# Kernel optimization log

Hardware: AMD Instinct MI355X
Metric: run time of the kernel (lower is better)

Reference implementation:

```python
import jax, jax.numpy as jnp
import numpy as np

ATTN_MULT = 8.0
NEG_INF = float('-inf')

N, Q, S, D = 16, 2048, 2048, 64


def setup_inputs() -> dict:
    key = jax.random.key(0)
    kq, kk, kv, kp = jax.random.split(key, 4)
    return {
        "queries_nqd": jax.random.normal(kq, (N, Q, D), dtype=jnp.float32),
        "keys_nsd": jax.random.normal(kk, (N, S, D), dtype=jnp.float32),
        "values_nsv": jax.random.normal(kv, (N, S, D), dtype=jnp.float32),
        "prefix_len_n": jax.random.randint(kp, (N,), 0, S, dtype=jnp.int64 if jax.config.jax_enable_x64 else jnp.int32),
    }


def reference(queries_nqd, keys_nsd, values_nsv, prefix_len_n):
    # attention_type == 'block_diagonal', backend == 'torch', dropout p == 0
    n, q, d = queries_nqd.shape
    s = keys_nsd.shape[1]
    scale = ATTN_MULT / d
    # prefix-block mask: key position < prefix_len (broadcast over queries)
    block_mask_n1s = (jnp.arange(s)[None, None, :] < prefix_len_n[:, None, None])  # [n,1,s]
    diag_mask_qs = jnp.arange(q)[:, None] == jnp.arange(s)[None, :]                # [q,s]
    mask_nqs = block_mask_n1s | diag_mask_qs[None, :, :]                           # [n,q,s]
    scores_nqs = jnp.einsum('nqd,nsd->nqs', queries_nqd, keys_nsd) * scale
    scores_nqs = jnp.where(mask_nqs, scores_nqs, NEG_INF)
    probs_nqs = jax.nn.softmax(scores_nqs, axis=-1)
    return jnp.einsum('nqs,nsv->nqv', probs_nqs, values_nsv)
```

## Files before the change

kernel.cpp:

```cpp
#include <hip/hip_runtime.h>
#include <hip/hip_bf16.h>
#include <math.h>

#define NH 16
#define QL 2048
#define SL 2048
#define DD 64
#define PSTR 72
#define QK_SCALE_LOG2E 0.1803368801111f

typedef __attribute__((ext_vector_type(8))) short short8;
typedef __attribute__((ext_vector_type(4))) float floatx4;
typedef __attribute__((ext_vector_type(4))) unsigned short ushort4v;
typedef __attribute__((ext_vector_type(8))) unsigned short ushort8v;

__device__ __forceinline__ unsigned short f2bf(float x) {
    unsigned u = __float_as_uint(x);
    u += 0x7FFFu + ((u >> 16) & 1u);
    return (unsigned short)(u >> 16);
}
__device__ __forceinline__ unsigned int f2bf2u(float x, float y) {
    __hip_bfloat162 h = __float22bfloat162_rn(make_float2(x, y));
    return *(unsigned int*)&h;
}
__device__ __forceinline__ float bf2f(unsigned short h) {
    return __uint_as_float((unsigned)h << 16);
}

__device__ __forceinline__ void gld16(const unsigned short* g, unsigned short* l) {
    __builtin_amdgcn_global_load_lds(
        (const __attribute__((address_space(1))) unsigned int*)g,
        (__attribute__((address_space(3))) unsigned int*)l, 16, 0, 0);
}

__global__ __launch_bounds__(256) void prep(
    const float* __restrict__ Kf, const float* __restrict__ Vf,
    unsigned short* __restrict__ Kb, unsigned short* __restrict__ Vtb)
{
    if (blockIdx.y == 0) {
        int idx = blockIdx.x * 256 + threadIdx.x;
        float4 v = ((const float4*)Kf)[idx];
        ushort4v h = { f2bf(v.x), f2bf(v.y), f2bf(v.z), f2bf(v.w) };
        *(ushort4v*)(Kb + (size_t)idx * 4) = h;
    } else {
        if (blockIdx.x >= 512) return;
        __shared__ unsigned short sT[64][PSTR];
        int bx = blockIdx.x;
        int n = bx >> 5, stile = bx & 31, s0 = stile * 64;
        int tid = (int)threadIdx.x;
        const float* vb = Vf + ((size_t)n * SL + s0) * DD;
        #pragma unroll
        for (int i = 0; i < 4; ++i) {
            int idx = tid + i * 256;
            int r = idx >> 4, c = (idx & 15) << 2;
            float4 v = *(const float4*)(vb + r * DD + c);
            sT[c + 0][r] = f2bf(v.x);
            sT[c + 1][r] = f2bf(v.y);
            sT[c + 2][r] = f2bf(v.z);
            sT[c + 3][r] = f2bf(v.w);
        }
        __syncthreads();
        int d = tid >> 2, sg = tid & 3;
        unsigned short* out = Vtb + (size_t)n * DD * SL + (size_t)d * SL + s0 + sg * 16;
        ushort8v a, b;
        #pragma unroll
        for (int i = 0; i < 8; ++i) { a[i] = sT[d][sg * 16 + i]; b[i] = sT[d][sg * 16 + 8 + i]; }
        *(ushort8v*)(out) = a;
        *(ushort8v*)(out + 8) = b;
    }
}

__global__ __launch_bounds__(256, 4) void attn_mfma_split(
    const float* __restrict__ Qf, const unsigned short* __restrict__ Kb,
    const unsigned short* __restrict__ Vtb, const int* __restrict__ plen_g,
    unsigned short* __restrict__ Opb, float* __restrict__ Lp, int spl)
{
    __shared__ unsigned short sK[2][64 * 64];
    __shared__ unsigned short sVt[2][64 * 64];
    __shared__ unsigned short sP[4 * 16 * 64];

    const int blk = blockIdx.x;
    const int n  = blk & (NH - 1);
    const int qt = blk >> 4;
    const int q0 = qt * 64;
    const int sp = blockIdx.y;
    const int sbeg = sp * spl;
    const int plen = plen_g[n];
    const int ntile = spl >> 6;
    const bool hasdiag = (q0 >= sbeg) && (q0 < sbeg + spl);
    if (!((sbeg < plen) || hasdiag)) return;

    const int tid  = (int)threadIdx.x;
    const int wave = tid >> 6, lane = tid & 63, quad = lane >> 4, l16 = lane & 15;

    int rem  = plen - sbeg;
    int base = (rem > 0) ? min((rem + 63) >> 6, ntile) : 0;
    int td   = hasdiag ? ((q0 - sbeg) >> 6) : -1;
    int total = base + ((td >= base) ? 1 : 0);

    const int qrow  = wave * 16 + l16;
    const int qglob = q0 + qrow;
    const int pmask = (l16 & 7) * 8;

    short8 bQ0, bQ1;
    {
        const float* qf = Qf + ((size_t)(n * QL + qglob)) * DD + quad * 8;
        float4 a0 = *(const float4*)(qf);
        float4 a1 = *(const float4*)(qf + 4);
        float4 c0 = *(const float4*)(qf + 32);
        float4 c1 = *(const float4*)(qf + 36);
        const float S = QK_SCALE_LOG2E;
        unsigned int u0[4] = {
            f2bf2u(a0.x * S, a0.y * S), f2bf2u(a0.z * S, a0.w * S),
            f2bf2u(a1.x * S, a1.y * S), f2bf2u(a1.z * S, a1.w * S) };
        unsigned int u1[4] = {
            f2bf2u(c0.x * S, c0.y * S), f2bf2u(c0.z * S, c0.w * S),
            f2bf2u(c1.x * S, c1.y * S), f2bf2u(c1.z * S, c1.w * S) };
        bQ0 = *(short8*)u0;
        bQ1 = *(short8*)u1;
    }

    const unsigned short* kh = Kb  + (size_t)n * SL * DD;
    const unsigned short* vh = Vtb + (size_t)n * DD * SL;

    const int seg0 = wave * 2, seg1 = wave * 2 + 1;
    const int r0 = seg0 * 8 + (lane >> 3), r1 = seg1 * 8 + (lane >> 3);
    const int cg0 = ((lane & 7) ^ (r0 & 7)) * 8, cg1 = ((lane & 7) ^ (r1 & 7)) * 8;

    {
        int t0 = (0 < base) ? 0 : td;
        const unsigned short* kg = kh + (size_t)(sbeg + t0 * 64) * DD;
        const unsigned short* vg = vh + (sbeg + t0 * 64);
        gld16(kg + r0 * DD + cg0, sK[0] + seg0 * 512);
        gld16(kg + r1 * DD + cg1, sK[0] + seg1 * 512);
        gld16(vg + (size_t)r0 * SL + cg0, sVt[0] + seg0 * 512);
        gld16(vg + (size_t)r1 * SL + cg1, sVt[0] + seg1 * 512);
    }

    floatx4 acc[4];
    #pragma unroll
    for (int dt = 0; dt < 4; ++dt) acc[dt] = (floatx4){0.f, 0.f, 0.f, 0.f};
    float lsum = 0.f;
    unsigned short* pw = sP + qrow * 64;

    for (int i = 0; i < total; ++i) {
        __syncthreads();

        if (i + 1 < total) {
            int tn = (i + 1 < base) ? (i + 1) : td;
            const unsigned short* kg = kh + (size_t)(sbeg + tn * 64) * DD;
            const unsigned short* vg = vh + (sbeg + tn * 64);
            unsigned short* dk = sK[(i + 1) & 1];
            unsigned short* dv = sVt[(i + 1) & 1];
            gld16(kg + r0 * DD + cg0, dk + seg0 * 512);
            gld16(kg + r1 * DD + cg1, dk + seg1 * 512);
            gld16(vg + (size_t)r0 * SL + cg0, dv + seg0 * 512);
            gld16(vg + (size_t)r1 * SL + cg1, dv + seg1 * 512);
        }

        const unsigned short* sk = sK[i & 1];
        const unsigned short* sv = sVt[i & 1];
        const int t  = (i < base) ? i : td;
        const int s0 = sbeg + t * 64;

        floatx4 sf[4];
        #pragma unroll
        for (int st2 = 0; st2 < 4; ++st2) sf[st2] = (floatx4){0.f, 0.f, 0.f, 0.f};
        #pragma unroll
        for (int st2 = 0; st2 < 4; ++st2) {
            int krow = st2 * 16 + l16;
            short8 aK0 = *(const short8*)(sk + krow * 64 + (((0 * 4 + quad) ^ (krow & 7)) * 8));
            short8 aK1 = *(const short8*)(sk + krow * 64 + (((1 * 4 + quad) ^ (krow & 7)) * 8));
            sf[st2] = __builtin_amdgcn_mfma_f32_16x16x32_bf16(aK0, bQ0, sf[st2], 0, 0, 0);
            sf[st2] = __builtin_amdgcn_mfma_f32_16x16x32_bf16(aK1, bQ1, sf[st2], 0, 0, 0);
        }

        if (s0 + 64 <= plen) {
            #pragma unroll
            for (int st2 = 0; st2 < 4; ++st2) {
                float p0 = __builtin_amdgcn_exp2f(sf[st2][0]);
                float p1 = __builtin_amdgcn_exp2f(sf[st2][1]);
                float p2 = __builtin_amdgcn_exp2f(sf[st2][2]);
                float p3 = __builtin_amdgcn_exp2f(sf[st2][3]);
                lsum += (p0 + p1) + (p2 + p3);
                uint2 pk = { f2bf2u(p0, p1), f2bf2u(p2, p3) };
                *(uint2*)(pw + ((st2 * 16 + quad * 4) ^ pmask)) = pk;
            }
        } else {
            #pragma unroll
            for (int st2 = 0; st2 < 4; ++st2) {
                float p[4];
                #pragma unroll
                for (int r = 0; r < 4; ++r) {
                    int s = s0 + st2 * 16 + quad * 4 + r;
                    bool valid = (s < plen) || (s == qglob);
                    p[r] = __builtin_amdgcn_exp2f(valid ? sf[st2][r] : -INFINITY);
                    lsum += p[r];
                }
                uint2 pk = { f2bf2u(p[0], p[1]), f2bf2u(p[2], p[3]) };
                *(uint2*)(pw + ((st2 * 16 + quad * 4) ^ pmask)) = pk;
            }
        }

        #pragma unroll
        for (int ks = 0; ks < 2; ++ks) {
            short8 aP = *(const short8*)(pw + ((ks * 32 + quad * 8) ^ pmask));
            #pragma unroll
            for (int dt = 0; dt < 4; ++dt) {
                int vrow = dt * 16 + l16;
                short8 bV = *(const short8*)(sv + vrow * 64 + (((ks * 4 + quad) ^ (vrow & 7)) * 8));
                acc[dt] = __builtin_amdgcn_mfma_f32_16x16x32_bf16(aP, bV, acc[dt], 0, 0, 0);
            }
        }
    }

    lsum += __shfl_xor(lsum, 16, 64);
    lsum += __shfl_xor(lsum, 32, 64);
    if (quad == 0)
        Lp[((size_t)sp * NH + n) * QL + q0 + qrow] = lsum;

    unsigned short* pws = sP + wave * 16 * 64;
    #pragma unroll
    for (int dt = 0; dt < 4; ++dt) {
        int chunk = dt * 2 + (l16 >> 3);
        #pragma unroll
        for (int r = 0; r < 4; ++r) {
            int row = quad * 4 + r;
            int sw = ((chunk ^ (row & 7)) * 8) + (l16 & 7);
            pws[row * 64 + sw] = f2bf(acc[dt][r]);
        }
    }
    const size_t qbase = ((size_t)sp * NH + n) * QL + q0 + wave * 16;
    #pragma unroll
    for (int t = 0; t < 2; ++t) {
        int row = t * 8 + (lane >> 3);
        int chunk = lane & 7;
        int sw = (chunk ^ (row & 7)) * 8;
        ushort8v val = *(const ushort8v*)(pws + row * 64 + sw);
        *(ushort8v*)(Opb + (qbase + row) * DD + chunk * 8) = val;
    }
}

__global__ __launch_bounds__(256) void combine(
    const unsigned short* __restrict__ Opb, const float* __restrict__ Lp,
    const int* __restrict__ plen_g, float* __restrict__ Og, int nsplit, int spl)
{
    int idx = blockIdx.x * 256 + (int)threadIdx.x;
    int d4 = idx & 15;
    int q  = (idx >> 4) & (QL - 1);
    int n  = idx >> 15;
    int plen = plen_g[n];
    int spd = q / spl;
    float4 s = {0.f, 0.f, 0.f, 0.f};
    float l = 0.f;
    for (int sp = 0; sp < nsplit; ++sp) {
        if ((sp * spl < plen) || (sp == spd)) {
            const unsigned short* ob = Opb + (((size_t)sp * NH + n) * QL + q) * DD + d4 * 4;
            ushort4v v = *(const ushort4v*)(ob);
            s.x += bf2f(v[0]); s.y += bf2f(v[1]); s.z += bf2f(v[2]); s.w += bf2f(v[3]);
            l += Lp[((size_t)sp * NH + n) * QL + q];
        }
    }
    float inv = 1.0f / l;
    float4 o = { s.x * inv, s.y * inv, s.z * inv, s.w * inv };
    *(float4*)(Og + ((size_t)n * QL + q) * DD + d4 * 4) = o;
}

extern "C" void kernel_launch(void* const* d_in, const int* in_sizes, int n_in,
                              void* d_out, int out_size, void* d_ws, size_t ws_size,
                              hipStream_t stream) {
    const float* Qf   = (const float*)d_in[0];
    const float* Kf   = (const float*)d_in[1];
    const float* Vf   = (const float*)d_in[2];
    const int*   plen = (const int*)d_in[3];
    float* Og = (float*)d_out;

    char* ws = (char*)d_ws;
    unsigned short* Kb  = (unsigned short*)(ws);
    unsigned short* Vtb = (unsigned short*)(ws + (4u << 20));
    unsigned short* Opb = (unsigned short*)(ws + (8u << 20));

    const size_t op_bytes = (size_t)NH * QL * DD * 2;
    const size_t lp_bytes = (size_t)NH * QL * 4;
    int nsplit = 1;
    if (ws_size >= (8u << 20) + 4 * (op_bytes + lp_bytes)) nsplit = 4;
    else if (ws_size >= (8u << 20) + 2 * (op_bytes + lp_bytes)) nsplit = 2;
    float* Lp = (float*)(ws + (8u << 20) + (size_t)nsplit * op_bytes);
    int spl = SL / nsplit;

    prep<<<dim3(2048, 2), 256, 0, stream>>>(Kf, Vf, Kb, Vtb);
    attn_mfma_split<<<dim3(NH * (QL / 64), nsplit), 256, 0, stream>>>(Qf, Kb, Vtb, plen, Opb, Lp, spl);
    combine<<<2048, 256, 0, stream>>>(Opb, Lp, plen, Og, nsplit, spl);
}
```

Before: 111.5 us.

## Widen attention query tile to 128 rows with 8 waves sharing K/V tiles

Each block now handles 128 query rows with 512 threads (8 waves), so every K/V tile staged in shared memory is reused by twice as many queries, halving global K/V traffic per query. Since a 128-row block spans two diagonal key tiles, the tile schedule is generalized to up to two diagonal tiles via a tile_of lambda. Each wave now loads one 8-row segment instead of two. Risks include fewer blocks (less parallelism for the masked/early-exit load balance), one extra diagonal tile per block, and higher register/occupancy pressure under the new launch bounds.

```diff
diff --git a/kernel.cpp b/kernel.cpp
--- a/kernel.cpp
+++ b/kernel.cpp
@@ -6,6 +6,7 @@
 #define QL 2048
 #define SL 2048
 #define DD 64
+#define BQ 128
 #define PSTR 72
 #define QK_SCALE_LOG2E 0.1803368801111f
 
@@ -70,19 +71,19 @@
     }
 }
 
-__global__ __launch_bounds__(256, 4) void attn_mfma_split(
+__global__ __launch_bounds__(512, 6) void attn_mfma_split(
     const float* __restrict__ Qf, const unsigned short* __restrict__ Kb,
     const unsigned short* __restrict__ Vtb, const int* __restrict__ plen_g,
     unsigned short* __restrict__ Opb, float* __restrict__ Lp, int spl)
 {
     __shared__ unsigned short sK[2][64 * 64];
     __shared__ unsigned short sVt[2][64 * 64];
-    __shared__ unsigned short sP[4 * 16 * 64];
+    __shared__ unsigned short sP[8 * 16 * 64];
 
     const int blk = blockIdx.x;
     const int n  = blk & (NH - 1);
     const int qt = blk >> 4;
-    const int q0 = qt * 64;
+    const int q0 = qt * BQ;
     const int sp = blockIdx.y;
     const int sbeg = sp * spl;
     const int plen = plen_g[n];
@@ -95,8 +96,13 @@
 
     int rem  = plen - sbeg;
     int base = (rem > 0) ? min((rem + 63) >> 6, ntile) : 0;
-    int td   = hasdiag ? ((q0 - sbeg) >> 6) : -1;
-    int total = base + ((td >= base) ? 1 : 0);
+    int td0 = -1, td1 = -1;
+    if (hasdiag) {
+        int d0 = (q0 - sbeg) >> 6;
+        if (d0 >= base) td0 = d0;
+        if (d0 + 1 >= base) td1 = d0 + 1;
+    }
+    const int total = base + (td0 >= 0) + (td1 >= 0);
 
     const int qrow  = wave * 16 + l16;
     const int qglob = q0 + qrow;
@@ -123,18 +129,21 @@
     const unsigned short* kh = Kb  + (size_t)n * SL * DD;
     const unsigned short* vh = Vtb + (size_t)n * DD * SL;
 
-    const int seg0 = wave * 2, seg1 = wave * 2 + 1;
-    const int r0 = seg0 * 8 + (lane >> 3), r1 = seg1 * 8 + (lane >> 3);
-    const int cg0 = ((lane & 7) ^ (r0 & 7)) * 8, cg1 = ((lane & 7) ^ (r1 & 7)) * 8;
+    const int rr = wave * 8 + (lane >> 3);
+    const int cg = ((lane & 7) ^ (rr & 7)) * 8;
+
+    auto tile_of = [&](int i) -> int {
+        if (i < base) return i;
+        if (i == base) return (td0 >= 0) ? td0 : td1;
+        return td1;
+    };
 
     {
-        int t0 = (0 < base) ? 0 : td;
+        int t0 = tile_of(0);
         const unsigned short* kg = kh + (size_t)(sbeg + t0 * 64) * DD;
         const unsigned short* vg = vh + (sbeg + t0 * 64);
-        gld16(kg + r0 * DD + cg0, sK[0] + seg0 * 512);
-        gld16(kg + r1 * DD + cg1, sK[0] + seg1 * 512);
-        gld16(vg + (size_t)r0 * SL + cg0, sVt[0] + seg0 * 512);
-        gld16(vg + (size_t)r1 * SL + cg1, sVt[0] + seg1 * 512);
+        gld16(kg + rr * DD + cg, sK[0] + wave * 512);
+        gld16(vg + (size_t)rr * SL + cg, sVt[0] + wave * 512);
     }
 
     floatx4 acc[4];
@@ -147,20 +156,16 @@
         __syncthreads();
 
         if (i + 1 < total) {
-            int tn = (i + 1 < base) ? (i + 1) : td;
+            int tn = tile_of(i + 1);
             const unsigned short* kg = kh + (size_t)(sbeg + tn * 64) * DD;
             const unsigned short* vg = vh + (sbeg + tn * 64);
-            unsigned short* dk = sK[(i + 1) & 1];
-            unsigned short* dv = sVt[(i + 1) & 1];
-            gld16(kg + r0 * DD + cg0, dk + seg0 * 512);
-            gld16(kg + r1 * DD + cg1, dk + seg1 * 512);
-            gld16(vg + (size_t)r0 * SL + cg0, dv + seg0 * 512);
-            gld16(vg + (size_t)r1 * SL + cg1, dv + seg1 * 512);
+            gld16(kg + rr * DD + cg, sK[(i + 1) & 1] + wave * 512);
+            gld16(vg + (size_t)rr * SL + cg, sVt[(i + 1) & 1] + wave * 512);
         }
 
         const unsigned short* sk = sK[i & 1];
         const unsigned short* sv = sVt[i & 1];
-        const int t  = (i < base) ? i : td;
+        const int t  = tile_of(i);
         const int s0 = sbeg + t * 64;
 
         floatx4 sf[4];
@@ -289,6 +294,6 @@
     int spl = SL / nsplit;
 
     prep<<<dim3(2048, 2), 256, 0, stream>>>(Kf, Vf, Kb, Vtb);
-    attn_mfma_split<<<dim3(NH * (QL / 64), nsplit), 256, 0, stream>>>(Qf, Kb, Vtb, plen, Opb, Lp, spl);
+    attn_mfma_split<<<dim3(NH * (QL / BQ), nsplit), 512, 0, stream>>>(Qf, Kb, Vtb, plen, Opb, Lp, spl);
     combine<<<2048, 256, 0, stream>>>(Opb, Lp, plen, Og, nsplit, spl);
 }
```

After: 110.0 us (median of 2 runs). Within noise of the previous version (-1.4%).
